# Performance work log

Measured on AMD Instinct MI355X. Metric: run time of the kernel, lower is better.

Reference implementation:

```python
import jax, jax.numpy as jnp
import numpy as np

B, N, D_IN, D_HID, D_OUT = 8, 512, 4608, 4608, 1152
DROP = 0.1
INV_SQRT2 = 0.7071067811865476
INV_SQRT_2PI = 0.3989422804014327


def _clean(s):
    # nan -> 1e-5, inf -> 1.0 (matches torch.where chain)
    return jnp.where(jnp.isnan(s), jnp.asarray(1e-5, s.dtype),
                     jnp.where(jnp.isinf(s), jnp.asarray(1.0, s.dtype), s))


def kl_regularizer(w_mu, w_sigma):
    d = w_mu.shape[0]
    ws = jax.nn.softplus(w_sigma)  # log(1+exp(w_sigma))
    return 0.5 * jnp.mean(d * ws + jnp.sum(w_mu * w_mu, axis=0) - d - d * jnp.log(ws))


def vdp_linear(mu_in, Sigma_in, w_mu, w_sigma):
    mu_out = jnp.matmul(mu_in, w_mu)                                 # [B,N,U]
    kl = kl_regularizer(w_mu, w_sigma)
    W_Sigma = jax.nn.softplus(w_sigma)                               # [U]
    Sigma_1 = jnp.matmul(Sigma_in, w_mu * w_mu)                      # w^T Sigma_in w (diag)
    Sigma_2 = jnp.sum(mu_in * mu_in, axis=-1, keepdims=True) * W_Sigma
    Sigma_3 = jnp.sum(Sigma_in, axis=-1, keepdims=True) * W_Sigma
    return mu_out, _clean(Sigma_1 + Sigma_2 + Sigma_3), kl


def vdp_gelu(mu_in, Sigma_in):
    # exact (erf) gelu and its analytic derivative: Phi(x) + x*phi(x)
    cdf = 0.5 * (1.0 + jax.lax.erf(mu_in * INV_SQRT2))
    pdf = jnp.exp(-0.5 * mu_in * mu_in) * INV_SQRT_2PI
    grad = cdf + mu_in * pdf
    return mu_in * cdf, grad * grad * Sigma_in


def vdp_dropout(mu_in, Sigma_in, mask):
    keep = 1.0 - DROP
    m = mask.astype(mu_in.dtype)
    mu_out = mu_in * m / keep                       # torch F.dropout scaling
    Sigma_out = Sigma_in * m / mu_in.shape[-1]      # kept Sigma values (unscaled), / units
    return mu_out, _clean(Sigma_out)


def setup_inputs() -> dict:
    key = jax.random.key(0)
    k = jax.random.split(key, 8)
    mu_in = jax.random.normal(k[0], (B, N, D_IN), dtype=jnp.float32)
    sigma_in = jax.random.uniform(k[1], (B, N, D_IN), dtype=jnp.float32)
    mask1 = jax.random.bernoulli(k[2], 1.0 - DROP, (B, N, D_HID))
    mask2 = jax.random.bernoulli(k[3], 1.0 - DROP, (B, N, D_OUT))
    w_mu1 = 0.05 * jax.random.normal(k[4], (D_IN, D_HID), dtype=jnp.float32)
    w_sigma1 = jnp.full((D_HID,), -4.6, dtype=jnp.float32)
    w_mu2 = 0.05 * jax.random.normal(k[5], (D_HID, D_OUT), dtype=jnp.float32)
    w_sigma2 = jnp.full((D_OUT,), -4.6, dtype=jnp.float32)
    return {"mu_in": mu_in, "sigma_in": sigma_in, "mask1": mask1, "mask2": mask2,
            "w_mu1": w_mu1, "w_sigma1": w_sigma1, "w_mu2": w_mu2, "w_sigma2": w_sigma2}


def reference(mu_in, sigma_in, mask1, mask2, w_mu1, w_sigma1, w_mu2, w_sigma2):
    mu, sig, kl1 = vdp_linear(mu_in, sigma_in, w_mu1, w_sigma1)
    mu, sig = vdp_gelu(mu, sig)
    mu, sig = vdp_dropout(mu, sig, mask1)
    mu, sig, kl2 = vdp_linear(mu, sig, w_mu2, w_sigma2)
    mu, sig = vdp_dropout(mu, sig, mask2)
    return mu, _clean(sig), kl1 + kl2
```

## Files before the change

kernel.cpp:

```cpp
#include <hip/hip_runtime.h>
#include <cstdint>
#include <cstddef>

static constexpr int Mrows = 4096;
static constexpr int K1 = 4608;
static constexpr int N1 = 4608;
static constexpr int N2 = 1152;
static constexpr int NPART1 = (K1 / 64) * (N1 / 64);
static constexpr int NPART2 = (K1 / 64) * (N2 / 64);

typedef float  f32x4  __attribute__((ext_vector_type(4)));
typedef __bf16 bf16x8 __attribute__((ext_vector_type(8)));
typedef unsigned short u16x8 __attribute__((ext_vector_type(8)));

__device__ __forceinline__ unsigned short f2bf(float f) {
  unsigned int u = __float_as_uint(f);
  u += 0x7fffu + ((u >> 16) & 1u);
  return (unsigned short)(u >> 16);
}
__device__ __forceinline__ float bf2f(unsigned short h) {
  return __uint_as_float(((unsigned int)h) << 16);
}
__device__ __forceinline__ float cleanf(float s) {
  if (__builtin_isnan(s)) return 1e-5f;
  if (__builtin_isinf(s)) return 1.0f;
  return s;
}

__global__ __launch_bounds__(256) void prep_in(
    const float* __restrict__ mu, const float* __restrict__ sg,
    unsigned short* __restrict__ A1, unsigned short* __restrict__ As16,
    float* __restrict__ rmu2, float* __restrict__ rsg)
{
  const int row = blockIdx.x;
  const int tid = threadIdx.x;
  const float4* mup = (const float4*)(mu + (size_t)row * K1);
  const float4* sgp = (const float4*)(sg + (size_t)row * K1);
  ushort4* a1p = (ushort4*)(A1 + (size_t)row * K1);
  ushort4* asp = (ushort4*)(As16 + (size_t)row * K1);
  float smu = 0.f, ssg = 0.f;
  for (int j = tid; j < K1 / 4; j += 256) {
    float4 m4 = mup[j];
    float4 s4 = sgp[j];
    smu += m4.x*m4.x + m4.y*m4.y + m4.z*m4.z + m4.w*m4.w;
    ssg += s4.x + s4.y + s4.z + s4.w;
    a1p[j] = make_ushort4(f2bf(m4.x), f2bf(m4.y), f2bf(m4.z), f2bf(m4.w));
    asp[j] = make_ushort4(f2bf(s4.x), f2bf(s4.y), f2bf(s4.z), f2bf(s4.w));
  }
  __shared__ float red[2][4];
  for (int off = 32; off; off >>= 1) {
    smu += __shfl_down(smu, off);
    ssg += __shfl_down(ssg, off);
  }
  const int lane = tid & 63, wv = tid >> 6;
  if (!lane) { red[0][wv] = smu; red[1][wv] = ssg; }
  __syncthreads();
  if (tid == 0) {
    rmu2[row] = red[0][0] + red[0][1] + red[0][2] + red[0][3];
    rsg[row]  = red[1][0] + red[1][1] + red[1][2] + red[1][3];
  }
}

__global__ __launch_bounds__(256) void prep_w2x(
    const float* __restrict__ w1, const float* __restrict__ w2,
    unsigned short* __restrict__ B1t, unsigned short* __restrict__ B1sq,
    unsigned short* __restrict__ B2t, unsigned short* __restrict__ B2sq,
    float* __restrict__ part1, float* __restrict__ part2)
{
  const int ybl = blockIdx.y;
  const bool is2 = ybl >= (N1 / 64);
  const int nb = is2 ? (ybl - N1 / 64) : ybl;
  const float* w = is2 ? w2 : w1;
  unsigned short* Bt = is2 ? B2t : B1t;
  unsigned short* Bq = is2 ? B2sq : B1sq;
  float* parts = is2 ? part2 : part1;
  const int N = is2 ? N2 : N1;

  const int kt = blockIdx.x * 64;
  const int nt = nb * 64;
  const int tid = threadIdx.x;

  __shared__ float t[64][65];
  float loc = 0.f;
  {
    const int r = tid >> 4;
    const int c = (tid & 15) * 4;
#pragma unroll
    for (int p = 0; p < 4; ++p) {
      const int k = p * 16 + r;
      float4 v = *(const float4*)(w + (size_t)(kt + k) * N + nt + c);
      t[k][c] = v.x; t[k][c + 1] = v.y; t[k][c + 2] = v.z; t[k][c + 3] = v.w;
      loc += v.x*v.x + v.y*v.y + v.z*v.z + v.w*v.w;
    }
  }
  __syncthreads();
  {
    const int kk = (tid & 7) * 8;
#pragma unroll
    for (int q = 0; q < 2; ++q) {
      const int n = (tid >> 3) + q * 32;
      u16x8 bt, bq;
#pragma unroll
      for (int i = 0; i < 8; ++i) {
        float v = t[kk + i][n];
        bt[i] = f2bf(v);
        bq[i] = f2bf(v * v);
      }
      size_t o = (size_t)(nt + n) * K1 + (kt + kk);
      *(u16x8*)(Bt + o) = bt;
      *(u16x8*)(Bq + o) = bq;
    }
  }
  __shared__ float red[4];
  for (int off = 32; off; off >>= 1) loc += __shfl_down(loc, off);
  const int lane = tid & 63, wv = tid >> 6;
  if (!lane) red[wv] = loc;
  __syncthreads();
  if (tid == 0)
    parts[nb * (K1 / 64) + blockIdx.x] = red[0] + red[1] + red[2] + red[3];
}

__global__ __launch_bounds__(256) void kl_prep(
    const float* __restrict__ wsig1, const float* __restrict__ wsig2,
    const float* __restrict__ part1, const float* __restrict__ part2,
    float* __restrict__ ws1, float* __restrict__ ws2, float* __restrict__ outkl)
{
  const int tid = threadIdx.x;
  float s1 = 0.f, l1 = 0.f, s2 = 0.f, l2 = 0.f, q1 = 0.f, q2 = 0.f;
  for (int j = tid; j < N1; j += 256) {
    float x = wsig1[j];
    float sp = (x > 20.f) ? x : log1pf(expf(x));
    ws1[j] = sp; s1 += sp; l1 += logf(sp);
  }
  for (int j = tid; j < N2; j += 256) {
    float x = wsig2[j];
    float sp = (x > 20.f) ? x : log1pf(expf(x));
    ws2[j] = sp; s2 += sp; l2 += logf(sp);
  }
  for (int j = tid; j < NPART1; j += 256) q1 += part1[j];
  for (int j = tid; j < NPART2; j += 256) q2 += part2[j];
  __shared__ float red[6][4];
  for (int off = 32; off; off >>= 1) {
    s1 += __shfl_down(s1, off); l1 += __shfl_down(l1, off);
    s2 += __shfl_down(s2, off); l2 += __shfl_down(l2, off);
    q1 += __shfl_down(q1, off); q2 += __shfl_down(q2, off);
  }
  const int lane = tid & 63, wv = tid >> 6;
  if (!lane) {
    red[0][wv] = s1; red[1][wv] = l1; red[2][wv] = s2;
    red[3][wv] = l2; red[4][wv] = q1; red[5][wv] = q2;
  }
  __syncthreads();
  if (tid == 0) {
    float S1v = red[0][0] + red[0][1] + red[0][2] + red[0][3];
    float L1v = red[1][0] + red[1][1] + red[1][2] + red[1][3];
    float S2v = red[2][0] + red[2][1] + red[2][2] + red[2][3];
    float L2v = red[3][0] + red[3][1] + red[3][2] + red[3][3];
    float Q1v = red[4][0] + red[4][1] + red[4][2] + red[4][3];
    float Q2v = red[5][0] + red[5][1] + red[5][2] + red[5][3];
    const float d = 4608.f;
    float kl1 = 0.5f * (d * (S1v / (float)N1) + Q1v / (float)N1 - d - d * (L1v / (float)N1));
    float kl2 = 0.5f * (d * (S2v / (float)N2) + Q2v / (float)N2 - d - d * (L2v / (float)N2));
    outkl[0] = kl1 + kl2;
  }
}

#define GLD16(gp, lp) __builtin_amdgcn_global_load_lds( \
    (__attribute__((address_space(1))) void*)(unsigned short*)(gp), \
    (__attribute__((address_space(3))) void*)(lp), 16, 0, 0)

__device__ __forceinline__ void storeC(float v, float* p) { *p = v; }
__device__ __forceinline__ void storeC(float v, unsigned short* p) { *p = f2bf(v); }

template <int NT, typename CT, bool FUSE>
__global__ __launch_bounds__(512, 4) void gemm256(
    const unsigned short* __restrict__ Amu, const unsigned short* __restrict__ Asg,
    const unsigned short* __restrict__ Bmu, const unsigned short* __restrict__ Bsq,
    CT* __restrict__ Cmu, CT* __restrict__ Csg,
    const int* __restrict__ mask2, const float* __restrict__ ws2,
    const float* __restrict__ r2mu, const float* __restrict__ r2sg)
{
  __shared__ __align__(16) char smem[81920];
  char* lA = smem;

  const int tid  = threadIdx.x;
  const int lane = tid & 63;
  const int wave = tid >> 6;
  const int which = blockIdx.z;
  const unsigned short* Ag = which ? Asg : Amu;
  const unsigned short* Bg = which ? Bsq : Bmu;
  CT* Cg = which ? Csg : Cmu;

  const int m0 = blockIdx.y * 128;
  const int n0 = blockIdx.x * 192;
  const int wm = (wave >> 2) * 64;
  const int wn = (wave & 3) * 48;
  const int fm = lane & 15;
  const int kq = lane >> 4;

  const int rbase = tid >> 3;
  const int gg = (tid & 7) ^ (rbase & 7);
  const unsigned short* gA0 = Ag + (size_t)(m0 + rbase) * K1 + gg * 8;
  const unsigned short* gB0 = Bg + (size_t)(n0 + rbase) * K1 + gg * 8;

  auto stA = [&](int buf, int part, int kt2) {
    const unsigned short* g = gA0 + (size_t)part * 64 * K1 + (size_t)kt2 * 64;
    char* l = lA + buf * 16384 + part * 8192 + tid * 16;
    GLD16(g, l);
  };
  auto stB = [&](int buf, int kt2) {
    const unsigned short* g = gB0 + (size_t)kt2 * 64;
    char* l = smem + 32768 + buf * 24576 + tid * 16;
    GLD16(g, l);
    GLD16(g + (size_t)64 * K1, l + 8192);
    GLD16(g + (size_t)128 * K1, l + 16384);
  };

  const int abase = (wm + fm) * 128;
  const int bbase = 32768 + (wn + fm) * 128;
  const int x0 = ((0 * 4 + kq) ^ (fm & 7)) * 16;
  const int x1 = ((1 * 4 + kq) ^ (fm & 7)) * 16;

  f32x4 acc[4][3];
#pragma unroll
  for (int i = 0; i < 4; ++i)
#pragma unroll
    for (int j = 0; j < 3; ++j) acc[i][j] = (f32x4){0.f, 0.f, 0.f, 0.f};

  stB(0, 0);
  stA(0, 0, 0); stA(0, 1, 0);
  stB(1, 1);
  asm volatile("s_waitcnt vmcnt(3)" ::: "memory");
  __builtin_amdgcn_s_barrier();

  const int ksteps = K1 / 64;
  for (int kt = 0; kt < ksteps; ++kt) {
    const int cur = kt & 1;
    const char* cA = lA + cur * 16384 + abase;
    const char* cB = smem + cur * 24576 + bbase;

    bf16x8 Af[4][2], Bf[3][2];

#pragma unroll
    for (int j = 0; j < 3; ++j) {
      Bf[j][0] = *(const bf16x8*)(cB + j * 2048 + x0);
      Bf[j][1] = *(const bf16x8*)(cB + j * 2048 + x1);
    }
#pragma unroll
    for (int i = 0; i < 2; ++i) {
      Af[i][0] = *(const bf16x8*)(cA + i * 2048 + x0);
      Af[i][1] = *(const bf16x8*)(cA + i * 2048 + x1);
    }
    if (kt + 1 < ksteps) stA(cur ^ 1, 0, kt + 1);
    asm volatile("s_waitcnt lgkmcnt(4)" ::: "memory");
    __builtin_amdgcn_s_barrier();
    asm volatile("s_waitcnt lgkmcnt(0)" ::: "memory");
    __builtin_amdgcn_s_setprio(1);
#pragma unroll
    for (int i = 0; i < 2; ++i)
#pragma unroll
      for (int j = 0; j < 2; ++j) {
        acc[i][j] = __builtin_amdgcn_mfma_f32_16x16x32_bf16(Af[i][0], Bf[j][0], acc[i][j], 0, 0, 0);
        acc[i][j] = __builtin_amdgcn_mfma_f32_16x16x32_bf16(Af[i][1], Bf[j][1], acc[i][j], 0, 0, 0);
      }
    __builtin_amdgcn_s_setprio(0);
    __builtin_amdgcn_s_barrier();

#pragma unroll
    for (int i = 2; i < 4; ++i) {
      Af[i][0] = *(const bf16x8*)(cA + i * 2048 + x0);
      Af[i][1] = *(const bf16x8*)(cA + i * 2048 + x1);
    }
    if (kt + 1 < ksteps) stA(cur ^ 1, 1, kt + 1);
    __builtin_amdgcn_s_barrier();
    asm volatile("s_waitcnt lgkmcnt(0)" ::: "memory");
    __builtin_amdgcn_s_setprio(1);
#pragma unroll
    for (int i = 2; i < 4; ++i)
#pragma unroll
      for (int j = 0; j < 2; ++j) {
        acc[i][j] = __builtin_amdgcn_mfma_f32_16x16x32_bf16(Af[i][0], Bf[j][0], acc[i][j], 0, 0, 0);
        acc[i][j] = __builtin_amdgcn_mfma_f32_16x16x32_bf16(Af[i][1], Bf[j][1], acc[i][j], 0, 0, 0);
      }
    __builtin_amdgcn_s_setprio(0);
    __builtin_amdgcn_s_barrier();

    if (kt + 2 < ksteps) stB(cur, kt + 2);
    __builtin_amdgcn_s_barrier();
    __builtin_amdgcn_s_setprio(1);
#pragma unroll
    for (int i = 0; i < 4; ++i) {
      acc[i][2] = __builtin_amdgcn_mfma_f32_16x16x32_bf16(Af[i][0], Bf[2][0], acc[i][2], 0, 0, 0);
      acc[i][2] = __builtin_amdgcn_mfma_f32_16x16x32_bf16(Af[i][1], Bf[2][1], acc[i][2], 0, 0, 0);
    }
    __builtin_amdgcn_s_setprio(0);
    if (kt < ksteps - 2) asm volatile("s_waitcnt vmcnt(3)" ::: "memory");
    else                 asm volatile("s_waitcnt vmcnt(0)" ::: "memory");
    __builtin_amdgcn_s_barrier();
  }

  const int rr = (lane >> 4) * 4;
  const int cc = lane & 15;
  if constexpr (!FUSE) {
#pragma unroll
    for (int i = 0; i < 4; ++i) {
      const int grow = m0 + wm + i * 16 + rr;
#pragma unroll
      for (int j = 0; j < 3; ++j) {
        const int gcol = n0 + wn + j * 16 + cc;
        CT* cp = Cg + (size_t)grow * NT + gcol;
#pragma unroll
        for (int r = 0; r < 4; ++r) storeC(acc[i][j][r], cp + (size_t)r * NT);
      }
    }
  } else {
    const float inv_keep  = 1.f / 0.9f;
    const float inv_units = 1.f / 1152.f;
    float wcol[3];
    if (which) {
#pragma unroll
      for (int j = 0; j < 3; ++j) wcol[j] = ws2[n0 + wn + j * 16 + cc];
    }
#pragma unroll
    for (int i = 0; i < 4; ++i) {
#pragma unroll
      for (int r = 0; r < 4; ++r) {
        const int grow = m0 + wm + i * 16 + rr + r;
        const float rterm = which ? (r2mu[grow] + r2sg[grow]) : 0.f;
#pragma unroll
        for (int j = 0; j < 3; ++j) {
          const int gcol = n0 + wn + j * 16 + cc;
          const float mm = (float)mask2[(size_t)grow * NT + gcol];
          const float v = acc[i][j][r];
          float o;
          if (which == 0) {
            o = v * mm * inv_keep;
          } else {
            float sig4 = cleanf(v + rterm * wcol[j]);
            o = cleanf(cleanf(sig4 * mm * inv_units));
          }
          Cg[(size_t)grow * NT + gcol] = (CT)o;
        }
      }
    }
  }
}

__global__ __launch_bounds__(256) void mid_kernel(
    const unsigned short* __restrict__ mu1, const unsigned short* __restrict__ S1,
    const int* __restrict__ mask1, const float* __restrict__ ws1,
    const float* __restrict__ rmu2, const float* __restrict__ rsg,
    unsigned short* __restrict__ A2, unsigned short* __restrict__ As2,
    float* __restrict__ r2mu, float* __restrict__ r2sg)
{
  const int row = blockIdx.x;
  const int tid = threadIdx.x;
  const float rterm = rmu2[row] + rsg[row];
  const ushort4* mup = (const ushort4*)(mu1 + (size_t)row * N1);
  const ushort4* s1p = (const ushort4*)(S1 + (size_t)row * N1);
  const int4* mkp = (const int4*)(mask1 + (size_t)row * N1);
  const float4* wsp = (const float4*)ws1;
  ushort4* a2p = (ushort4*)(A2 + (size_t)row * N1);
  ushort4* as2p = (ushort4*)(As2 + (size_t)row * N1);
  float smu = 0.f, ssg = 0.f;
  for (int j = tid; j < N1 / 4; j += 256) {
    ushort4 m4 = mup[j]; ushort4 s4 = s1p[j]; int4 k4 = mkp[j]; float4 w4 = wsp[j];
    float xv[4] = {bf2f(m4.x), bf2f(m4.y), bf2f(m4.z), bf2f(m4.w)};
    float Sv[4] = {bf2f(s4.x), bf2f(s4.y), bf2f(s4.z), bf2f(s4.w)};
    float wv[4] = {w4.x, w4.y, w4.z, w4.w};
    int   kv[4] = {k4.x, k4.y, k4.z, k4.w};
    unsigned short oa[4], os[4];
#pragma unroll
    for (int t = 0; t < 4; t++) {
      float sig1 = cleanf(Sv[t] + rterm * wv[t]);
      float x = xv[t];
      float cdf = 0.5f * (1.f + erff(x * 0.70710678118654752f));
      float pdf = expf(-0.5f * x * x) * 0.3989422804014327f;
      float g = cdf + x * pdf;
      float mu2v = x * cdf;
      float sig2 = g * g * sig1;
      float mm = (float)kv[t];
      float mu3 = mu2v * mm * (1.f / 0.9f);
      float sig3 = cleanf(sig2 * mm * (1.f / 4608.f));
      smu += mu3 * mu3;
      ssg += sig3;
      oa[t] = f2bf(mu3);
      os[t] = f2bf(sig3);
    }
    a2p[j] = make_ushort4(oa[0], oa[1], oa[2], oa[3]);
    as2p[j] = make_ushort4(os[0], os[1], os[2], os[3]);
  }
  __shared__ float red[2][4];
  for (int off = 32; off; off >>= 1) {
    smu += __shfl_down(smu, off);
    ssg += __shfl_down(ssg, off);
  }
  const int lane = tid & 63, wv2 = tid >> 6;
  if (!lane) { red[0][wv2] = smu; red[1][wv2] = ssg; }
  __syncthreads();
  if (tid == 0) {
    r2mu[row] = red[0][0] + red[0][1] + red[0][2] + red[0][3];
    r2sg[row] = red[1][0] + red[1][1] + red[1][2] + red[1][3];
  }
}

extern "C" void kernel_launch(void* const* d_in, const int* in_sizes, int n_in,
                              void* d_out, int out_size, void* d_ws, size_t ws_size,
                              hipStream_t stream)
{
  const float* mu_in = (const float*)d_in[0];
  const float* sg_in = (const float*)d_in[1];
  const int* mask1 = (const int*)d_in[2];
  const int* mask2 = (const int*)d_in[3];
  const float* w_mu1 = (const float*)d_in[4];
  const float* wsig1 = (const float*)d_in[5];
  const float* w_mu2 = (const float*)d_in[6];
  const float* wsig2 = (const float*)d_in[7];
  float* out = (float*)d_out;

  char* ws = (char*)d_ws;
  const size_t oA1  = 0;
  const size_t oAs  = oA1  + (size_t)37748736;
  const size_t oB1t = oAs  + (size_t)37748736;
  const size_t oB1q = oB1t + (size_t)42467328;
  const size_t oB2t = oB1q + (size_t)42467328;
  const size_t oB2q = oB2t + (size_t)10616832;
  const size_t oMu1 = oB2q + (size_t)10616832;
  const size_t oS1  = oMu1 + (size_t)37748736;
  const size_t oVec = oS1  + (size_t)37748736;

  unsigned short* A1     = (unsigned short*)(ws + oA1);
  unsigned short* As16   = (unsigned short*)(ws + oAs);
  unsigned short* B1t    = (unsigned short*)(ws + oB1t);
  unsigned short* B1sq16 = (unsigned short*)(ws + oB1q);
  unsigned short* B2t    = (unsigned short*)(ws + oB2t);
  unsigned short* B2sq16 = (unsigned short*)(ws + oB2q);
  unsigned short* mu1b   = (unsigned short*)(ws + oMu1);
  unsigned short* S1b16  = (unsigned short*)(ws + oS1);

  float* rmu2 = (float*)(ws + oVec);
  float* rsg  = rmu2 + Mrows;
  float* r2mu = rsg + Mrows;
  float* r2sg = r2mu + Mrows;
  float* ws1v = r2sg + Mrows;
  float* ws2v = ws1v + N1;
  float* part1 = ws2v + N2;
  float* part2 = part1 + NPART1;

  prep_in<<<Mrows, 256, 0, stream>>>(mu_in, sg_in, A1, As16, rmu2, rsg);
  prep_w2x<<<dim3(K1 / 64, N1 / 64 + N2 / 64), 256, 0, stream>>>(
      w_mu1, w_mu2, B1t, B1sq16, B2t, B2sq16, part1, part2);
  kl_prep<<<1, 256, 0, stream>>>(wsig1, wsig2, part1, part2, ws1v, ws2v,
                                 out + (size_t)2 * Mrows * N2);

  gemm256<N1, unsigned short, false><<<dim3(N1 / 192, Mrows / 128, 2), 512, 0, stream>>>(
      A1, As16, B1t, B1sq16, mu1b, S1b16, nullptr, nullptr, nullptr, nullptr);

  mid_kernel<<<Mrows, 256, 0, stream>>>(mu1b, S1b16, mask1, ws1v, rmu2, rsg,
                                        A1, As16, r2mu, r2sg);

  gemm256<N2, float, true><<<dim3(N2 / 192, Mrows / 128, 2), 512, 0, stream>>>(
      A1, As16, B2t, B2sq16, out, out + (size_t)Mrows * N2,
      mask2, ws2v, r2mu, r2sg);

  (void)in_sizes; (void)n_in; (void)out_size; (void)ws_size;
}
```

Baseline: 793.6 us.

## Compute variance GEMMs in scaled FP8 and remap workgroup order

The variance path (Sigma_in times w^2) now runs in FP8 with fixed power-of-two scales, which halves operand bytes and uses FP8 MFMA instructions for half of the GEMM work. The mean path stays in bf16. The GEMM kernel also remaps the linear workgroup id with a stride-8 interleave, which changes how tiles map to XCDs for cache locality. The risk is precision: FP8 with static scales can underflow or saturate on the variance terms.

New measurement: 832.2 us. 4.9% more time.

```diff
diff --git a/kernel.cpp b/kernel.cpp
--- a/kernel.cpp
+++ b/kernel.cpp
@@ -9,6 +9,12 @@
 static constexpr int NPART1 = (K1 / 64) * (N1 / 64);
 static constexpr int NPART2 = (K1 / 64) * (N2 / 64);
 
+static constexpr float SC_SIGIN = 256.f;
+static constexpr float SC_WSQ   = 4096.f;
+static constexpr float SC_SIG3  = 16384.f;
+static constexpr float DSC_L1   = 1.f / (SC_SIGIN * SC_WSQ);
+static constexpr float DSC_L2   = 1.f / (SC_SIG3 * SC_WSQ);
+
 typedef float  f32x4  __attribute__((ext_vector_type(4)));
 typedef __bf16 bf16x8 __attribute__((ext_vector_type(8)));
 typedef unsigned short u16x8 __attribute__((ext_vector_type(8)));
@@ -26,10 +32,15 @@
   if (__builtin_isinf(s)) return 1.0f;
   return s;
 }
+__device__ __forceinline__ unsigned int pk_fp8x4(float a, float b, float c, float d) {
+  int p = __builtin_amdgcn_cvt_pk_fp8_f32(a, b, 0, false);
+  p = __builtin_amdgcn_cvt_pk_fp8_f32(c, d, p, true);
+  return (unsigned int)p;
+}
 
 __global__ __launch_bounds__(256) void prep_in(
     const float* __restrict__ mu, const float* __restrict__ sg,
-    unsigned short* __restrict__ A1, unsigned short* __restrict__ As16,
+    unsigned short* __restrict__ A1, unsigned char* __restrict__ As8,
     float* __restrict__ rmu2, float* __restrict__ rsg)
 {
   const int row = blockIdx.x;
@@ -37,7 +48,7 @@
   const float4* mup = (const float4*)(mu + (size_t)row * K1);
   const float4* sgp = (const float4*)(sg + (size_t)row * K1);
   ushort4* a1p = (ushort4*)(A1 + (size_t)row * K1);
-  ushort4* asp = (ushort4*)(As16 + (size_t)row * K1);
+  unsigned int* asp = (unsigned int*)(As8 + (size_t)row * K1);
   float smu = 0.f, ssg = 0.f;
   for (int j = tid; j < K1 / 4; j += 256) {
     float4 m4 = mup[j];
@@ -45,7 +56,7 @@
     smu += m4.x*m4.x + m4.y*m4.y + m4.z*m4.z + m4.w*m4.w;
     ssg += s4.x + s4.y + s4.z + s4.w;
     a1p[j] = make_ushort4(f2bf(m4.x), f2bf(m4.y), f2bf(m4.z), f2bf(m4.w));
-    asp[j] = make_ushort4(f2bf(s4.x), f2bf(s4.y), f2bf(s4.z), f2bf(s4.w));
+    asp[j] = pk_fp8x4(s4.x * SC_SIGIN, s4.y * SC_SIGIN, s4.z * SC_SIGIN, s4.w * SC_SIGIN);
   }
   __shared__ float red[2][4];
   for (int off = 32; off; off >>= 1) {
@@ -63,8 +74,8 @@
 
 __global__ __launch_bounds__(256) void prep_w2x(
     const float* __restrict__ w1, const float* __restrict__ w2,
-    unsigned short* __restrict__ B1t, unsigned short* __restrict__ B1sq,
-    unsigned short* __restrict__ B2t, unsigned short* __restrict__ B2sq,
+    unsigned short* __restrict__ B1t, unsigned char* __restrict__ B1q,
+    unsigned short* __restrict__ B2t, unsigned char* __restrict__ B2q,
     float* __restrict__ part1, float* __restrict__ part2)
 {
   const int ybl = blockIdx.y;
@@ -72,7 +83,7 @@
   const int nb = is2 ? (ybl - N1 / 64) : ybl;
   const float* w = is2 ? w2 : w1;
   unsigned short* Bt = is2 ? B2t : B1t;
-  unsigned short* Bq = is2 ? B2sq : B1sq;
+  unsigned char*  Bq = is2 ? B2q : B1q;
   float* parts = is2 ? part2 : part1;
   const int N = is2 ? N2 : N1;
 
@@ -99,16 +110,18 @@
 #pragma unroll
     for (int q = 0; q < 2; ++q) {
       const int n = (tid >> 3) + q * 32;
-      u16x8 bt, bq;
+      u16x8 bt;
+      float qv[8];
 #pragma unroll
       for (int i = 0; i < 8; ++i) {
         float v = t[kk + i][n];
         bt[i] = f2bf(v);
-        bq[i] = f2bf(v * v);
+        qv[i] = v * v * SC_WSQ;
       }
       size_t o = (size_t)(nt + n) * K1 + (kt + kk);
       *(u16x8*)(Bt + o) = bt;
-      *(u16x8*)(Bq + o) = bq;
+      *(unsigned int*)(Bq + o)     = pk_fp8x4(qv[0], qv[1], qv[2], qv[3]);
+      *(unsigned int*)(Bq + o + 4) = pk_fp8x4(qv[4], qv[5], qv[6], qv[7]);
     }
   }
   __shared__ float red[4];
@@ -166,7 +179,7 @@
 }
 
 #define GLD16(gp, lp) __builtin_amdgcn_global_load_lds( \
-    (__attribute__((address_space(1))) void*)(unsigned short*)(gp), \
+    (__attribute__((address_space(1))) void*)(gp), \
     (__attribute__((address_space(3))) void*)(lp), 16, 0, 0)
 
 __device__ __forceinline__ void storeC(float v, float* p) { *p = v; }
@@ -174,11 +187,12 @@
 
 template <int NT, typename CT, bool FUSE>
 __global__ __launch_bounds__(512, 4) void gemm256(
-    const unsigned short* __restrict__ Amu, const unsigned short* __restrict__ Asg,
-    const unsigned short* __restrict__ Bmu, const unsigned short* __restrict__ Bsq,
+    const unsigned short* __restrict__ Amu, const unsigned char* __restrict__ As8,
+    const unsigned short* __restrict__ Bmu, const unsigned char* __restrict__ Bq8,
     CT* __restrict__ Cmu, CT* __restrict__ Csg,
     const int* __restrict__ mask2, const float* __restrict__ ws2,
-    const float* __restrict__ r2mu, const float* __restrict__ r2sg)
+    const float* __restrict__ r2mu, const float* __restrict__ r2sg,
+    float sdescale)
 {
   __shared__ __align__(16) char smem[81920];
   char* lA = smem;
@@ -186,13 +200,17 @@
   const int tid  = threadIdx.x;
   const int lane = tid & 63;
   const int wave = tid >> 6;
-  const int which = blockIdx.z;
-  const unsigned short* Ag = which ? Asg : Amu;
-  const unsigned short* Bg = which ? Bsq : Bmu;
-  CT* Cg = which ? Csg : Cmu;
-
-  const int m0 = blockIdx.y * 128;
-  const int n0 = blockIdx.x * 192;
+
+  int lid = blockIdx.x + gridDim.x * (blockIdx.y + gridDim.y * blockIdx.z);
+  const int nwg = gridDim.x * gridDim.y * gridDim.z;
+  lid = (lid & 7) * (nwg >> 3) + (lid >> 3);
+  const int bx = lid % gridDim.x;
+  const int tq = lid / gridDim.x;
+  const int by = tq % gridDim.y;
+  const int which = tq / gridDim.y;
+
+  const int m0 = by * 128;
+  const int n0 = bx * 192;
   const int wm = (wave >> 2) * 64;
   const int wn = (wave & 3) * 48;
   const int fm = lane & 15;
@@ -200,26 +218,9 @@
 
   const int rbase = tid >> 3;
   const int gg = (tid & 7) ^ (rbase & 7);
-  const unsigned short* gA0 = Ag + (size_t)(m0 + rbase) * K1 + gg * 8;
-  const unsigned short* gB0 = Bg + (size_t)(n0 + rbase) * K1 + gg * 8;
-
-  auto stA = [&](int buf, int part, int kt2) {
-    const unsigned short* g = gA0 + (size_t)part * 64 * K1 + (size_t)kt2 * 64;
-    char* l = lA + buf * 16384 + part * 8192 + tid * 16;
-    GLD16(g, l);
-  };
-  auto stB = [&](int buf, int kt2) {
-    const unsigned short* g = gB0 + (size_t)kt2 * 64;
-    char* l = smem + 32768 + buf * 24576 + tid * 16;
-    GLD16(g, l);
-    GLD16(g + (size_t)64 * K1, l + 8192);
-    GLD16(g + (size_t)128 * K1, l + 16384);
-  };
 
   const int abase = (wm + fm) * 128;
   const int bbase = 32768 + (wn + fm) * 128;
-  const int x0 = ((0 * 4 + kq) ^ (fm & 7)) * 16;
-  const int x1 = ((1 * 4 + kq) ^ (fm & 7)) * 16;
 
   f32x4 acc[4][3];
 #pragma unroll
@@ -227,78 +228,192 @@
 #pragma unroll
     for (int j = 0; j < 3; ++j) acc[i][j] = (f32x4){0.f, 0.f, 0.f, 0.f};
 
-  stB(0, 0);
-  stA(0, 0, 0); stA(0, 1, 0);
-  stB(1, 1);
-  asm volatile("s_waitcnt vmcnt(3)" ::: "memory");
-  __builtin_amdgcn_s_barrier();
-
-  const int ksteps = K1 / 64;
-  for (int kt = 0; kt < ksteps; ++kt) {
-    const int cur = kt & 1;
-    const char* cA = lA + cur * 16384 + abase;
-    const char* cB = smem + cur * 24576 + bbase;
-
-    bf16x8 Af[4][2], Bf[3][2];
-
-#pragma unroll
-    for (int j = 0; j < 3; ++j) {
-      Bf[j][0] = *(const bf16x8*)(cB + j * 2048 + x0);
-      Bf[j][1] = *(const bf16x8*)(cB + j * 2048 + x1);
-    }
-#pragma unroll
-    for (int i = 0; i < 2; ++i) {
-      Af[i][0] = *(const bf16x8*)(cA + i * 2048 + x0);
-      Af[i][1] = *(const bf16x8*)(cA + i * 2048 + x1);
-    }
-    if (kt + 1 < ksteps) stA(cur ^ 1, 0, kt + 1);
-    asm volatile("s_waitcnt lgkmcnt(4)" ::: "memory");
+  if (which == 0) {
+    const unsigned short* gA0 = Amu + (size_t)(m0 + rbase) * K1 + gg * 8;
+    const unsigned short* gB0 = Bmu + (size_t)(n0 + rbase) * K1 + gg * 8;
+
+    auto stA = [&](int buf, int part, int kt2) {
+      const unsigned short* g = gA0 + (size_t)part * 64 * K1 + (size_t)kt2 * 64;
+      GLD16(g, lA + buf * 16384 + part * 8192 + tid * 16);
+    };
+    auto stB = [&](int buf, int kt2) {
+      const unsigned short* g = gB0 + (size_t)kt2 * 64;
+      char* l = smem + 32768 + buf * 24576 + tid * 16;
+      GLD16(g, l);
+      GLD16(g + (size_t)64 * K1, l + 8192);
+      GLD16(g + (size_t)128 * K1, l + 16384);
+    };
+
+    const int x0 = ((0 * 4 + kq) ^ (fm & 7)) * 16;
+    const int x1 = ((1 * 4 + kq) ^ (fm & 7)) * 16;
+
+    stB(0, 0);
+    stA(0, 0, 0); stA(0, 1, 0);
+    stB(1, 1);
+    asm volatile("s_waitcnt vmcnt(3)" ::: "memory");
     __builtin_amdgcn_s_barrier();
-    asm volatile("s_waitcnt lgkmcnt(0)" ::: "memory");
-    __builtin_amdgcn_s_setprio(1);
-#pragma unroll
-    for (int i = 0; i < 2; ++i)
-#pragma unroll
-      for (int j = 0; j < 2; ++j) {
-        acc[i][j] = __builtin_amdgcn_mfma_f32_16x16x32_bf16(Af[i][0], Bf[j][0], acc[i][j], 0, 0, 0);
-        acc[i][j] = __builtin_amdgcn_mfma_f32_16x16x32_bf16(Af[i][1], Bf[j][1], acc[i][j], 0, 0, 0);
-      }
-    __builtin_amdgcn_s_setprio(0);
+
+    const int ksteps = K1 / 64;
+    for (int kt = 0; kt < ksteps; ++kt) {
+      const int cur = kt & 1;
+      const char* cA = lA + cur * 16384 + abase;
+      const char* cB = smem + cur * 24576 + bbase;
+
+      bf16x8 Af[4][2], Bf[3][2];
+
+#pragma unroll
+      for (int j = 0; j < 3; ++j) {
+        Bf[j][0] = *(const bf16x8*)(cB + j * 2048 + x0);
+        Bf[j][1] = *(const bf16x8*)(cB + j * 2048 + x1);
+      }
+#pragma unroll
+      for (int i = 0; i < 2; ++i) {
+        Af[i][0] = *(const bf16x8*)(cA + i * 2048 + x0);
+        Af[i][1] = *(const bf16x8*)(cA + i * 2048 + x1);
+      }
+      if (kt + 1 < ksteps) stA(cur ^ 1, 0, kt + 1);
+      asm volatile("s_waitcnt lgkmcnt(4)" ::: "memory");
+      __builtin_amdgcn_s_barrier();
+      asm volatile("s_waitcnt lgkmcnt(0)" ::: "memory");
+      __builtin_amdgcn_s_setprio(1);
+#pragma unroll
+      for (int i = 0; i < 2; ++i)
+#pragma unroll
+        for (int j = 0; j < 2; ++j) {
+          acc[i][j] = __builtin_amdgcn_mfma_f32_16x16x32_bf16(Af[i][0], Bf[j][0], acc[i][j], 0, 0, 0);
+          acc[i][j] = __builtin_amdgcn_mfma_f32_16x16x32_bf16(Af[i][1], Bf[j][1], acc[i][j], 0, 0, 0);
+        }
+      __builtin_amdgcn_s_setprio(0);
+      __builtin_amdgcn_s_barrier();
+
+#pragma unroll
+      for (int i = 2; i < 4; ++i) {
+        Af[i][0] = *(const bf16x8*)(cA + i * 2048 + x0);
+        Af[i][1] = *(const bf16x8*)(cA + i * 2048 + x1);
+      }
+      if (kt + 1 < ksteps) stA(cur ^ 1, 1, kt + 1);
+      __builtin_amdgcn_s_barrier();
+      asm volatile("s_waitcnt lgkmcnt(0)" ::: "memory");
+      __builtin_amdgcn_s_setprio(1);
+#pragma unroll
+      for (int i = 2; i < 4; ++i)
+#pragma unroll
+        for (int j = 0; j < 2; ++j) {
+          acc[i][j] = __builtin_amdgcn_mfma_f32_16x16x32_bf16(Af[i][0], Bf[j][0], acc[i][j], 0, 0, 0);
+          acc[i][j] = __builtin_amdgcn_mfma_f32_16x16x32_bf16(Af[i][1], Bf[j][1], acc[i][j], 0, 0, 0);
+        }
+      __builtin_amdgcn_s_setprio(0);
+      __builtin_amdgcn_s_barrier();
+
+      if (kt + 2 < ksteps) stB(cur, kt + 2);
+      __builtin_amdgcn_s_barrier();
+      __builtin_amdgcn_s_setprio(1);
+#pragma unroll
+      for (int i = 0; i < 4; ++i) {
+        acc[i][2] = __builtin_amdgcn_mfma_f32_16x16x32_bf16(Af[i][0], Bf[2][0], acc[i][2], 0, 0, 0);
+        acc[i][2] = __builtin_amdgcn_mfma_f32_16x16x32_bf16(Af[i][1], Bf[2][1], acc[i][2], 0, 0, 0);
+      }
+      __builtin_amdgcn_s_setprio(0);
+      if (kt < ksteps - 2) asm volatile("s_waitcnt vmcnt(3)" ::: "memory");
+      else                 asm volatile("s_waitcnt vmcnt(0)" ::: "memory");
+      __builtin_amdgcn_s_barrier();
+    }
+  } else {
+    const unsigned char* gA0 = As8 + (size_t)(m0 + rbase) * K1 + gg * 16;
+    const unsigned char* gB0 = Bq8 + (size_t)(n0 + rbase) * K1 + gg * 16;
+
+    auto stA = [&](int buf, int part, int kt2) {
+      const unsigned char* g = gA0 + (size_t)part * 64 * K1 + (size_t)kt2 * 128;
+      GLD16(g, lA + buf * 16384 + part * 8192 + tid * 16);
+    };
+    auto stB = [&](int buf, int kt2) {
+      const unsigned char* g = gB0 + (size_t)kt2 * 128;
+      char* l = smem + 32768 + buf * 24576 + tid * 16;
+      GLD16(g, l);
+      GLD16(g + (size_t)64 * K1, l + 8192);
+      GLD16(g + (size_t)128 * K1, l + 16384);
+    };
+
+    int xs8[4];
+#pragma unroll
+    for (int s = 0; s < 4; ++s)
+      xs8[s] = ((s * 2 + (kq >> 1)) ^ (fm & 7)) * 16 + (kq & 1) * 8;
+
+    stB(0, 0);
+    stA(0, 0, 0); stA(0, 1, 0);
+    stB(1, 1);
+    asm volatile("s_waitcnt vmcnt(3)" ::: "memory");
     __builtin_amdgcn_s_barrier();
 
-#pragma unroll
-    for (int i = 2; i < 4; ++i) {
-      Af[i][0] = *(const bf16x8*)(cA + i * 2048 + x0);
-      Af[i][1] = *(const bf16x8*)(cA + i * 2048 + x1);
-    }
-    if (kt + 1 < ksteps) stA(cur ^ 1, 1, kt + 1);
-    __builtin_amdgcn_s_barrier();
-    asm volatile("s_waitcnt lgkmcnt(0)" ::: "memory");
-    __builtin_amdgcn_s_setprio(1);
-#pragma unroll
-    for (int i = 2; i < 4; ++i)
-#pragma unroll
-      for (int j = 0; j < 2; ++j) {
-        acc[i][j] = __builtin_amdgcn_mfma_f32_16x16x32_bf16(Af[i][0], Bf[j][0], acc[i][j], 0, 0, 0);
-        acc[i][j] = __builtin_amdgcn_mfma_f32_16x16x32_bf16(Af[i][1], Bf[j][1], acc[i][j], 0, 0, 0);
-      }
-    __builtin_amdgcn_s_setprio(0);
-    __builtin_amdgcn_s_barrier();
-
-    if (kt + 2 < ksteps) stB(cur, kt + 2);
-    __builtin_amdgcn_s_barrier();
-    __builtin_amdgcn_s_setprio(1);
-#pragma unroll
-    for (int i = 0; i < 4; ++i) {
-      acc[i][2] = __builtin_amdgcn_mfma_f32_16x16x32_bf16(Af[i][0], Bf[2][0], acc[i][2], 0, 0, 0);
-      acc[i][2] = __builtin_amdgcn_mfma_f32_16x16x32_bf16(Af[i][1], Bf[2][1], acc[i][2], 0, 0, 0);
-    }
-    __builtin_amdgcn_s_setprio(0);
-    if (kt < ksteps - 2) asm volatile("s_waitcnt vmcnt(3)" ::: "memory");
-    else                 asm volatile("s_waitcnt vmcnt(0)" ::: "memory");
-    __builtin_amdgcn_s_barrier();
-  }
-
+    const int ksteps = K1 / 128;
+    for (int kt = 0; kt < ksteps; ++kt) {
+      const int cur = kt & 1;
+      const char* cA = lA + cur * 16384 + abase;
+      const char* cB = smem + cur * 24576 + bbase;
+
+      long Af8[4][4], Bf8[3][4];
+
+#pragma unroll
+      for (int j = 0; j < 3; ++j)
+#pragma unroll
+        for (int s = 0; s < 4; ++s)
+          Bf8[j][s] = *(const long*)(cB + j * 2048 + xs8[s]);
+#pragma unroll
+      for (int i = 0; i < 2; ++i)
+#pragma unroll
+        for (int s = 0; s < 4; ++s)
+          Af8[i][s] = *(const long*)(cA + i * 2048 + xs8[s]);
+      if (kt + 1 < ksteps) stA(cur ^ 1, 0, kt + 1);
+      asm volatile("s_waitcnt lgkmcnt(8)" ::: "memory");
+      __builtin_amdgcn_s_barrier();
+      asm volatile("s_waitcnt lgkmcnt(0)" ::: "memory");
+      __builtin_amdgcn_s_setprio(1);
+#pragma unroll
+      for (int i = 0; i < 2; ++i)
+#pragma unroll
+        for (int j = 0; j < 2; ++j)
+#pragma unroll
+          for (int s = 0; s < 4; ++s)
+            acc[i][j] = __builtin_amdgcn_mfma_f32_16x16x32_fp8_fp8(Af8[i][s], Bf8[j][s], acc[i][j], 0, 0, 0);
+      __builtin_amdgcn_s_setprio(0);
+      __builtin_amdgcn_s_barrier();
+
+#pragma unroll
+      for (int i = 2; i < 4; ++i)
+#pragma unroll
+        for (int s = 0; s < 4; ++s)
+          Af8[i][s] = *(const long*)(cA + i * 2048 + xs8[s]);
+      if (kt + 1 < ksteps) stA(cur ^ 1, 1, kt + 1);
+      __builtin_amdgcn_s_barrier();
+      asm volatile("s_waitcnt lgkmcnt(0)" ::: "memory");
+      __builtin_amdgcn_s_setprio(1);
+#pragma unroll
+      for (int i = 2; i < 4; ++i)
+#pragma unroll
+        for (int j = 0; j < 2; ++j)
+#pragma unroll
+          for (int s = 0; s < 4; ++s)
+            acc[i][j] = __builtin_amdgcn_mfma_f32_16x16x32_fp8_fp8(Af8[i][s], Bf8[j][s], acc[i][j], 0, 0, 0);
+      __builtin_amdgcn_s_setprio(0);
+      __builtin_amdgcn_s_barrier();
+
+      if (kt + 2 < ksteps) stB(cur, kt + 2);
+      __builtin_amdgcn_s_barrier();
+      __builtin_amdgcn_s_setprio(1);
+#pragma unroll
+      for (int i = 0; i < 4; ++i)
+#pragma unroll
+        for (int s = 0; s < 4; ++s)
+          acc[i][2] = __builtin_amdgcn_mfma_f32_16x16x32_fp8_fp8(Af8[i][s], Bf8[2][s], acc[i][2], 0, 0, 0);
+      __builtin_amdgcn_s_setprio(0);
+      if (kt < ksteps - 2) asm volatile("s_waitcnt vmcnt(3)" ::: "memory");
+      else                 asm volatile("s_waitcnt vmcnt(0)" ::: "memory");
+      __builtin_amdgcn_s_barrier();
+    }
+  }
+
+  CT* Cg = which ? Csg : Cmu;
+  const float dsc = which ? sdescale : 1.f;
   const int rr = (lane >> 4) * 4;
   const int cc = lane & 15;
   if constexpr (!FUSE) {
@@ -310,7 +425,7 @@
         const int gcol = n0 + wn + j * 16 + cc;
         CT* cp = Cg + (size_t)grow * NT + gcol;
 #pragma unroll
-        for (int r = 0; r < 4; ++r) storeC(acc[i][j][r], cp + (size_t)r * NT);
+        for (int r = 0; r < 4; ++r) storeC(acc[i][j][r] * dsc, cp + (size_t)r * NT);
       }
     }
   } else {
@@ -331,7 +446,7 @@
         for (int j = 0; j < 3; ++j) {
           const int gcol = n0 + wn + j * 16 + cc;
           const float mm = (float)mask2[(size_t)grow * NT + gcol];
-          const float v = acc[i][j][r];
+          const float v = acc[i][j][r] * dsc;
           float o;
           if (which == 0) {
             o = v * mm * inv_keep;
@@ -350,7 +465,7 @@
     const unsigned short* __restrict__ mu1, const unsigned short* __restrict__ S1,
     const int* __restrict__ mask1, const float* __restrict__ ws1,
     const float* __restrict__ rmu2, const float* __restrict__ rsg,
-    unsigned short* __restrict__ A2, unsigned short* __restrict__ As2,
+    unsigned short* __restrict__ A2, unsigned char* __restrict__ As2,
     float* __restrict__ r2mu, float* __restrict__ r2sg)
 {
   const int row = blockIdx.x;
@@ -361,7 +476,7 @@
   const int4* mkp = (const int4*)(mask1 + (size_t)row * N1);
   const float4* wsp = (const float4*)ws1;
   ushort4* a2p = (ushort4*)(A2 + (size_t)row * N1);
-  ushort4* as2p = (ushort4*)(As2 + (size_t)row * N1);
+  unsigned int* as2p = (unsigned int*)(As2 + (size_t)row * N1);
   float smu = 0.f, ssg = 0.f;
   for (int j = tid; j < N1 / 4; j += 256) {
     ushort4 m4 = mup[j]; ushort4 s4 = s1p[j]; int4 k4 = mkp[j]; float4 w4 = wsp[j];
@@ -369,7 +484,8 @@
     float Sv[4] = {bf2f(s4.x), bf2f(s4.y), bf2f(s4.z), bf2f(s4.w)};
     float wv[4] = {w4.x, w4.y, w4.z, w4.w};
     int   kv[4] = {k4.x, k4.y, k4.z, k4.w};
-    unsigned short oa[4], os[4];
+    unsigned short oa[4];
+    float os[4];
 #pragma unroll
     for (int t = 0; t < 4; t++) {
       float sig1 = cleanf(Sv[t] + rterm * wv[t]);
@@ -385,10 +501,10 @@
       smu += mu3 * mu3;
       ssg += sig3;
       oa[t] = f2bf(mu3);
-      os[t] = f2bf(sig3);
+      os[t] = sig3 * SC_SIG3;
     }
     a2p[j] = make_ushort4(oa[0], oa[1], oa[2], oa[3]);
-    as2p[j] = make_ushort4(os[0], os[1], os[2], os[3]);
+    as2p[j] = pk_fp8x4(os[0], os[1], os[2], os[3]);
   }
   __shared__ float red[2][4];
   for (int off = 32; off; off >>= 1) {
@@ -429,14 +545,14 @@
   const size_t oS1  = oMu1 + (size_t)37748736;
   const size_t oVec = oS1  + (size_t)37748736;
 
-  unsigned short* A1     = (unsigned short*)(ws + oA1);
-  unsigned short* As16   = (unsigned short*)(ws + oAs);
-  unsigned short* B1t    = (unsigned short*)(ws + oB1t);
-  unsigned short* B1sq16 = (unsigned short*)(ws + oB1q);
-  unsigned short* B2t    = (unsigned short*)(ws + oB2t);
-  unsigned short* B2sq16 = (unsigned short*)(ws + oB2q);
-  unsigned short* mu1b   = (unsigned short*)(ws + oMu1);
-  unsigned short* S1b16  = (unsigned short*)(ws + oS1);
+  unsigned short* A1    = (unsigned short*)(ws + oA1);
+  unsigned char*  As8   = (unsigned char*)(ws + oAs);
+  unsigned short* B1t   = (unsigned short*)(ws + oB1t);
+  unsigned char*  B1q8  = (unsigned char*)(ws + oB1q);
+  unsigned short* B2t   = (unsigned short*)(ws + oB2t);
+  unsigned char*  B2q8  = (unsigned char*)(ws + oB2q);
+  unsigned short* mu1b  = (unsigned short*)(ws + oMu1);
+  unsigned short* S1b16 = (unsigned short*)(ws + oS1);
 
   float* rmu2 = (float*)(ws + oVec);
   float* rsg  = rmu2 + Mrows;
@@ -447,21 +563,21 @@
   float* part1 = ws2v + N2;
   float* part2 = part1 + NPART1;
 
-  prep_in<<<Mrows, 256, 0, stream>>>(mu_in, sg_in, A1, As16, rmu2, rsg);
+  prep_in<<<Mrows, 256, 0, stream>>>(mu_in, sg_in, A1, As8, rmu2, rsg);
   prep_w2x<<<dim3(K1 / 64, N1 / 64 + N2 / 64), 256, 0, stream>>>(
-      w_mu1, w_mu2, B1t, B1sq16, B2t, B2sq16, part1, part2);
+      w_mu1, w_mu2, B1t, B1q8, B2t, B2q8, part1, part2);
   kl_prep<<<1, 256, 0, stream>>>(wsig1, wsig2, part1, part2, ws1v, ws2v,
                                  out + (size_t)2 * Mrows * N2);
 
   gemm256<N1, unsigned short, false><<<dim3(N1 / 192, Mrows / 128, 2), 512, 0, stream>>>(
-      A1, As16, B1t, B1sq16, mu1b, S1b16, nullptr, nullptr, nullptr, nullptr);
+      A1, As8, B1t, B1q8, mu1b, S1b16, nullptr, nullptr, nullptr, nullptr, DSC_L1);
 
   mid_kernel<<<Mrows, 256, 0, stream>>>(mu1b, S1b16, mask1, ws1v, rmu2, rsg,
-                                        A1, As16, r2mu, r2sg);
+                                        A1, As8, r2mu, r2sg);
 
   gemm256<N2, float, true><<<dim3(N2 / 192, Mrows / 128, 2), 512, 0, stream>>>(
-      A1, As16, B2t, B2sq16, out, out + (size_t)Mrows * N2,
-      mask2, ws2v, r2mu, r2sg);
+      A1, As8, B2t, B2q8, out, out + (size_t)Mrows * N2,
+      mask2, ws2v, r2mu, r2sg, DSC_L2);
 
   (void)in_sizes; (void)n_in; (void)out_size; (void)ws_size;
 }
```
